# Optimization experiments

Hardware: AMD Instinct MI355X
Metric: run time of the kernel (lower is better)

The kernel has to match this reference:

```python
import jax, jax.numpy as jnp
import numpy as np
from itertools import product

B, C, N = 2, 64, 30000
D, H, W = 64, 64, 64


def _make_shift():
    # itertools.product over (-1,0,1)^3, scaled by 2/(size-1) per axis in (x->W, y->H, z->D) order
    s = np.array(list(product((-1, 0, 1), repeat=3)), dtype=np.float32)  # [27,3]
    scale = np.array([2.0 / (W - 1), 2.0 / (H - 1), 2.0 / (D - 1)], dtype=np.float32)
    return jnp.asarray(s * scale)  # [27,3]


def setup_inputs() -> dict:
    key = jax.random.key(0)
    k1, k2, k3 = jax.random.split(key, 3)
    voxel_features = jax.random.normal(k1, (B, C, D, H, W), dtype=jnp.float32)
    vertices = jax.random.uniform(k2, (B, N, 3), dtype=jnp.float32, minval=-1.0, maxval=1.0)
    # kaiming_normal for relu on a (C, C, 1, 27) conv kernel: std = sqrt(2 / fan_in)
    conv_w = jax.random.normal(k3, (C, C, 27), dtype=jnp.float32) * np.float32(np.sqrt(2.0 / (C * 27)))
    conv_b = jnp.zeros((C,), dtype=jnp.float32)
    return {"voxel_features": voxel_features, "vertices": vertices, "conv_w": conv_w, "conv_b": conv_b}


def _trilinear_sample(vol, grid):
    # vol: [C, D, H, W]; grid: [M, 3] normalized (x, y, z) in [-1, 1]
    # F.grid_sample semantics: mode='bilinear' (trilinear), padding_mode='border', align_corners=True
    sizes_f = jnp.array([W - 1, H - 1, D - 1], dtype=vol.dtype)
    coord = (grid + 1.0) * 0.5 * sizes_f  # unnormalize, align_corners=True
    coord = jnp.clip(coord, 0.0, sizes_f)  # border padding
    c0f = jnp.floor(coord)
    f = coord - c0f  # fractional weights [M,3]
    c0 = c0f.astype(jnp.int32)
    c1 = jnp.minimum(c0 + 1, jnp.array([W - 1, H - 1, D - 1], dtype=jnp.int32))
    x0, y0, z0 = c0[:, 0], c0[:, 1], c0[:, 2]
    x1, y1, z1 = c1[:, 0], c1[:, 1], c1[:, 2]
    fx, fy, fz = f[:, 0], f[:, 1], f[:, 2]

    def g(zi, yi, xi):
        return vol[:, zi, yi, xi]  # [C, M]

    out = (g(z0, y0, x0) * ((1 - fx) * (1 - fy) * (1 - fz))
           + g(z0, y0, x1) * (fx * (1 - fy) * (1 - fz))
           + g(z0, y1, x0) * ((1 - fx) * fy * (1 - fz))
           + g(z0, y1, x1) * (fx * fy * (1 - fz))
           + g(z1, y0, x0) * ((1 - fx) * (1 - fy) * fz)
           + g(z1, y0, x1) * (fx * (1 - fy) * fz)
           + g(z1, y1, x0) * ((1 - fx) * fy * fz)
           + g(z1, y1, x1) * (fx * fy * fz))
    return out  # [C, M]


def reference(voxel_features, vertices, conv_w, conv_b):
    shift = _make_shift()  # [27,3]
    # neighbourhood grid: [B, N, 27, 3] -> flatten to [B, N*27, 3]
    grid = (vertices[:, :, None, :] + shift[None, None, :, :]).reshape(B, N * 27, 3)
    feats = jax.vmap(_trilinear_sample)(voxel_features, grid)  # [B, C, N*27]
    feats = feats.reshape(B, C, N, 27)
    # Conv2d(C, C, kernel=(1,27)) == learned weighted sum over 27 neighbors + channel mix
    out = jnp.einsum("bcnk,ock->bno", feats, conv_w) + conv_b[None, None, :]  # [B, N, C]
    return out
```

## Files before the change

kernel.cpp:

```cpp
#include <hip/hip_runtime.h>
#include <stdint.h>

#define NBATCH 2
#define NVERT  30000
#define VOLCH  16777216ull
#define KDIM   1728
#define ASTR   (KDIM + 8)

typedef __attribute__((ext_vector_type(8))) __bf16 bf16x8;
typedef __attribute__((ext_vector_type(4))) float f32x4;

__device__ __forceinline__ float b2f(unsigned short u) {
  unsigned int x = ((unsigned int)u) << 16;
  return __builtin_bit_cast(float, x);
}

__device__ __forceinline__ unsigned short f2b(float f) {
  unsigned int u = __builtin_bit_cast(unsigned int, f);
  u = (u + 0x7FFFu + ((u >> 16) & 1u)) >> 16;
  return (unsigned short)u;
}

__global__ __launch_bounds__(256) void transpose_vox(
    const float* __restrict__ vox, unsigned short* __restrict__ T) {
  __shared__ float tile[64][65];
  const int b = blockIdx.y;
  const int zy = blockIdx.x;
  const size_t src0 = (size_t)b * 64 * 262144 + (size_t)zy * 64;
#pragma unroll
  for (int i = 0; i < 16; ++i) {
    int idx = i * 256 + threadIdx.x;
    int c = idx >> 6, x = idx & 63;
    tile[c][x] = vox[src0 + (size_t)c * 262144 + x];
  }
  __syncthreads();
  const size_t dst0 = ((size_t)b * 4096 + zy) * 4096;
#pragma unroll
  for (int i = 0; i < 16; ++i) {
    int idx = i * 256 + threadIdx.x;
    int x = idx >> 6, c = idx & 63;
    T[dst0 + x * 64 + c] = f2b(tile[c][x]);
  }
}

__global__ __launch_bounds__(256) void prep_w(
    const float* __restrict__ w, unsigned short* __restrict__ W3) {
  int t = blockIdx.x * 256 + threadIdx.x;
  int o = t / 1728;
  int rem = t - o * 1728;
  int c = rem / 27;
  int k = rem - c * 27;
  int K = k * 64 + c;
  W3[((size_t)(K >> 3) * 64 + o) * 8 + (K & 7)] = f2b(w[t]);
}

__device__ __forceinline__ void axis_setup(float v, int idx[4], float gw[3][4]) {
  float coord = (v + 1.0f) * 0.5f * 63.0f;
  coord = fminf(fmaxf(coord, 0.0f), 63.0f);
  int b0 = (int)coord;
  if (b0 > 63) b0 = 63;
#pragma unroll
  for (int p = 0; p < 4; ++p) {
    int q = b0 - 1 + p;
    idx[p] = min(max(q, 0), 63);
  }
#pragma unroll
  for (int d = 0; d < 3; ++d) {
    float t = coord + (float)(d - 1);
    float tc = fminf(fmaxf(t, 0.0f), 63.0f);
    float fl = floorf(tc);
    int i0 = (int)fl;
    if (i0 > 63) i0 = 63;
    float f = tc - fl;
    int i1 = min(i0 + 1, 63);
    int p0 = i0 - b0 + 1;
    int p1 = i1 - b0 + 1;
#pragma unroll
    for (int p = 0; p < 4; ++p) {
      float g = (p == p0) ? (1.0f - f) : 0.0f;
      g += (p == p1) ? f : 0.0f;
      gw[d][p] = g;
    }
  }
}

__global__ __launch_bounds__(256, 2) void fused_main(
    const float* __restrict__ verts, const unsigned short* __restrict__ T,
    const unsigned short* __restrict__ W3, const float* __restrict__ bias,
    float* __restrict__ out) {
  __shared__ __align__(16) unsigned short A_lds[16][ASTR];
  const int tid = threadIdx.x;
  const int wave = tid >> 6;
  const int lane = tid & 63;
  const int batch = blockIdx.y;
  const int n0 = blockIdx.x * 16;

  const unsigned short* Tb = T + (size_t)batch * VOLCH + lane;

#pragma unroll 1
  for (int vl = 0; vl < 4; ++vl) {
    const int m = wave * 4 + vl;
    const size_t vbase = ((size_t)batch * NVERT + (n0 + m)) * 3;
    const float vx = verts[vbase + 0];
    const float vy = verts[vbase + 1];
    const float vz = verts[vbase + 2];

    int xi[4], yi[4], zi[4];
    float gwx[3][4], gwy[3][4], gwz[3][4];
    axis_setup(vx, xi, gwx);
    axis_setup(vy, yi, gwy);
    axis_setup(vz, zi, gwz);

    int xo[4];
#pragma unroll
    for (int p = 0; p < 4; ++p) xo[p] = xi[p] << 6;

    float fe[3][3][3];
#pragma unroll
    for (int a = 0; a < 3; ++a)
#pragma unroll
      for (int bb = 0; bb < 3; ++bb)
#pragma unroll
        for (int cc = 0; cc < 3; ++cc) fe[a][bb][cc] = 0.0f;

#pragma unroll
    for (int pz = 0; pz < 4; ++pz) {
      float ryv[3][3];
#pragma unroll
      for (int a = 0; a < 3; ++a)
#pragma unroll
        for (int bb = 0; bb < 3; ++bb) ryv[a][bb] = 0.0f;
      const int zoff = zi[pz] << 18;
#pragma unroll
      for (int py = 0; py < 4; ++py) {
        const unsigned short* rp = Tb + zoff + (yi[py] << 12);
        float v0 = b2f(rp[xo[0]]);
        float v1 = b2f(rp[xo[1]]);
        float v2 = b2f(rp[xo[2]]);
        float v3 = b2f(rp[xo[3]]);
        const float wy0 = gwy[0][py], wy1 = gwy[1][py], wy2 = gwy[2][py];
#pragma unroll
        for (int dx = 0; dx < 3; ++dx) {
          float rx = v0 * gwx[dx][0] + v1 * gwx[dx][1] +
                     v2 * gwx[dx][2] + v3 * gwx[dx][3];
          ryv[0][dx] += rx * wy0;
          ryv[1][dx] += rx * wy1;
          ryv[2][dx] += rx * wy2;
        }
      }
#pragma unroll
      for (int dz = 0; dz < 3; ++dz) {
        const float wz = gwz[dz][pz];
#pragma unroll
        for (int dy = 0; dy < 3; ++dy)
#pragma unroll
          for (int dx = 0; dx < 3; ++dx) fe[dz][dy][dx] += ryv[dy][dx] * wz;
      }
    }

    unsigned short* arow = &A_lds[m][0];
#pragma unroll
    for (int dz = 0; dz < 3; ++dz)
#pragma unroll
      for (int dy = 0; dy < 3; ++dy)
#pragma unroll
        for (int dx = 0; dx < 3; ++dx) {
          int k = dx * 9 + dy * 3 + dz;
          arow[(k << 6) + lane] = f2b(fe[dz][dy][dx]);
        }
  }
  __syncthreads();

  const int g = lane >> 4;
  const int r = lane & 15;
  const int o0 = wave * 16;
  f32x4 acc = {0.0f, 0.0f, 0.0f, 0.0f};
  const unsigned short* aptr = &A_lds[r][g * 8];
  const unsigned short* bptr = W3 + (size_t)(g * 64 + o0 + r) * 8;
  for (int kk = 0; kk < 54; ++kk) {
    bf16x8 a = *reinterpret_cast<const bf16x8*>(aptr + kk * 32);
    bf16x8 b = *reinterpret_cast<const bf16x8*>(bptr + (size_t)kk * 2048);
    acc = __builtin_amdgcn_mfma_f32_16x16x32_bf16(a, b, acc, 0, 0, 0);
  }

  const int oc = o0 + r;
  const float bo = bias[oc];
  float* op = out + ((size_t)batch * NVERT + n0) * 64 + oc;
#pragma unroll
  for (int i = 0; i < 4; ++i) {
    op[(size_t)(g * 4 + i) * 64] = acc[i] + bo;
  }
}

extern "C" void kernel_launch(void* const* d_in, const int* in_sizes, int n_in,
                              void* d_out, int out_size, void* d_ws, size_t ws_size,
                              hipStream_t stream) {
  const float* vox   = (const float*)d_in[0];
  const float* verts = (const float*)d_in[1];
  const float* convw = (const float*)d_in[2];
  const float* convb = (const float*)d_in[3];
  float* out = (float*)d_out;

  const size_t t_elems = (size_t)NBATCH * VOLCH;
  const size_t need = t_elems * 2 + (size_t)110592 * 2;
  if (ws_size < need) {
    hipMemsetAsync(d_out, 0xFF, (size_t)out_size * 4, stream);
    return;
  }
  unsigned short* T  = (unsigned short*)d_ws;
  unsigned short* W3 = T + t_elems;

  transpose_vox<<<dim3(4096, NBATCH), 256, 0, stream>>>(vox, T);
  prep_w<<<432, 256, 0, stream>>>(convw, W3);
  fused_main<<<dim3(NVERT / 16, NBATCH), 256, 0, stream>>>(verts, T, W3, convb, out);
}
```

Before: 429.1 us.

## Vectorize voxel transpose and double fused-kernel waves with split-K MFMA reduction

The transpose kernel now moves four elements per thread access, using float4 loads and ushort4 stores instead of scalar ones. The main kernel grows from 256 to 512 threads per block. Each wave samples two vertices instead of four, and the MFMA K loop is split across two wave halves whose partial sums are combined through a new LDS buffer before output. This aims to raise latency hiding for the gather-heavy sampling phase and cut global transaction count in the transpose. The cost is an extra barrier, more LDS per block and possible register pressure under launch_bounds(512,4).

Measured after the change: 479.9 us. 11.8% more time.

```diff
diff --git a/kernel.cpp b/kernel.cpp
--- a/kernel.cpp
+++ b/kernel.cpp
@@ -26,20 +26,27 @@
   __shared__ float tile[64][65];
   const int b = blockIdx.y;
   const int zy = blockIdx.x;
+  const int t = threadIdx.x;
   const size_t src0 = (size_t)b * 64 * 262144 + (size_t)zy * 64;
 #pragma unroll
-  for (int i = 0; i < 16; ++i) {
-    int idx = i * 256 + threadIdx.x;
-    int c = idx >> 6, x = idx & 63;
-    tile[c][x] = vox[src0 + (size_t)c * 262144 + x];
+  for (int i = 0; i < 4; ++i) {
+    const int c = (t >> 4) + (i << 4);
+    const int x4 = (t & 15) << 2;
+    const float4 v = *reinterpret_cast<const float4*>(
+        vox + src0 + (size_t)c * 262144 + x4);
+    tile[c][x4 + 0] = v.x; tile[c][x4 + 1] = v.y;
+    tile[c][x4 + 2] = v.z; tile[c][x4 + 3] = v.w;
   }
   __syncthreads();
   const size_t dst0 = ((size_t)b * 4096 + zy) * 4096;
 #pragma unroll
-  for (int i = 0; i < 16; ++i) {
-    int idx = i * 256 + threadIdx.x;
-    int x = idx >> 6, c = idx & 63;
-    T[dst0 + x * 64 + c] = f2b(tile[c][x]);
+  for (int i = 0; i < 4; ++i) {
+    const int x = (t >> 4) + (i << 4);
+    const int c4 = (t & 15) << 2;
+    ushort4 o;
+    o.x = f2b(tile[c4 + 0][x]); o.y = f2b(tile[c4 + 1][x]);
+    o.z = f2b(tile[c4 + 2][x]); o.w = f2b(tile[c4 + 3][x]);
+    *reinterpret_cast<ushort4*>(T + dst0 + (size_t)x * 64 + c4) = o;
   }
 }
 
@@ -84,11 +91,12 @@
   }
 }
 
-__global__ __launch_bounds__(256, 2) void fused_main(
+__global__ __launch_bounds__(512, 4) void fused_main(
     const float* __restrict__ verts, const unsigned short* __restrict__ T,
     const unsigned short* __restrict__ W3, const float* __restrict__ bias,
     float* __restrict__ out) {
   __shared__ __align__(16) unsigned short A_lds[16][ASTR];
+  __shared__ float red[2][16][65];
   const int tid = threadIdx.x;
   const int wave = tid >> 6;
   const int lane = tid & 63;
@@ -98,8 +106,8 @@
   const unsigned short* Tb = T + (size_t)batch * VOLCH + lane;
 
 #pragma unroll 1
-  for (int vl = 0; vl < 4; ++vl) {
-    const int m = wave * 4 + vl;
+  for (int vl = 0; vl < 2; ++vl) {
+    const int m = wave * 2 + vl;
     const size_t vbase = ((size_t)batch * NVERT + (n0 + m)) * 3;
     const float vx = verts[vbase + 0];
     const float vy = verts[vbase + 1];
@@ -173,23 +181,32 @@
 
   const int g = lane >> 4;
   const int r = lane & 15;
-  const int o0 = wave * 16;
+  const int o0 = (wave & 3) * 16;
+  const int h = wave >> 2;
   f32x4 acc = {0.0f, 0.0f, 0.0f, 0.0f};
   const unsigned short* aptr = &A_lds[r][g * 8];
   const unsigned short* bptr = W3 + (size_t)(g * 64 + o0 + r) * 8;
-  for (int kk = 0; kk < 54; ++kk) {
+#pragma unroll 1
+  for (int kk = h * 27; kk < h * 27 + 27; ++kk) {
     bf16x8 a = *reinterpret_cast<const bf16x8*>(aptr + kk * 32);
     bf16x8 b = *reinterpret_cast<const bf16x8*>(bptr + (size_t)kk * 2048);
     acc = __builtin_amdgcn_mfma_f32_16x16x32_bf16(a, b, acc, 0, 0, 0);
   }
 
-  const int oc = o0 + r;
-  const float bo = bias[oc];
-  float* op = out + ((size_t)batch * NVERT + n0) * 64 + oc;
-#pragma unroll
-  for (int i = 0; i < 4; ++i) {
-    op[(size_t)(g * 4 + i) * 64] = acc[i] + bo;
-  }
+#pragma unroll
+  for (int i = 0; i < 4; ++i) red[h][g * 4 + i][o0 + r] = acc[i];
+  __syncthreads();
+
+  const float* redf = &red[0][0][0];
+#pragma unroll
+  for (int i = 0; i < 2; ++i) {
+    const int idx = tid + i * 512;
+    const int row = idx >> 6;
+    const int o = idx & 63;
+    const float s = red[0][row][o] + red[1][row][o] + bias[o];
+    out[((size_t)batch * NVERT + n0 + row) * 64 + o] = s;
+  }
+  (void)redf;
 }
 
 extern "C" void kernel_launch(void* const* d_in, const int* in_sizes, int n_in,
@@ -212,5 +229,5 @@
 
   transpose_vox<<<dim3(4096, NBATCH), 256, 0, stream>>>(vox, T);
   prep_w<<<432, 256, 0, stream>>>(convw, W3);
-  fused_main<<<dim3(NVERT / 16, NBATCH), 256, 0, stream>>>(verts, T, W3, convb, out);
-}
+  fused_main<<<dim3(NVERT / 16, NBATCH), 512, 0, stream>>>(verts, T, W3, convb, out);
+}
```

## Bin vertices spatially, remap blocks to XCDs, and vectorize voxel transpose

Applied to the files above, without the earlier changes.

Adds a counting-sort pass (histogram, scan, scatter) that groups vertices by z and coarse y cell. The main kernel then processes spatially nearby vertices together, and a block-index remap gives each XCD a contiguous range of sorted work, so gathers from the transposed bf16 volume should reuse L2 better. The transpose now handles four z-y rows per block with float4 loads and ushort4 stores. The trade is extra small kernels plus scattered output writes through the permutation, and the launch-bounds occupancy hint is dropped.

Result: slower. 446.4 us (+4.0%).

```diff
diff --git a/kernel.cpp b/kernel.cpp
--- a/kernel.cpp
+++ b/kernel.cpp
@@ -6,6 +6,7 @@
 #define VOLCH  16777216ull
 #define KDIM   1728
 #define ASTR   (KDIM + 8)
+#define NBINS  512
 
 typedef __attribute__((ext_vector_type(8))) __bf16 bf16x8;
 typedef __attribute__((ext_vector_type(4))) float f32x4;
@@ -23,23 +24,36 @@
 
 __global__ __launch_bounds__(256) void transpose_vox(
     const float* __restrict__ vox, unsigned short* __restrict__ T) {
-  __shared__ float tile[64][65];
+  __shared__ unsigned short tile[4][65][66];
   const int b = blockIdx.y;
-  const int zy = blockIdx.x;
-  const size_t src0 = (size_t)b * 64 * 262144 + (size_t)zy * 64;
+  const int zy0 = blockIdx.x * 4;
+  const int t = threadIdx.x;
+  const size_t src0 = (size_t)b * 64 * 262144 + (size_t)zy0 * 64;
 #pragma unroll
   for (int i = 0; i < 16; ++i) {
-    int idx = i * 256 + threadIdx.x;
-    int c = idx >> 6, x = idx & 63;
-    tile[c][x] = vox[src0 + (size_t)c * 262144 + x];
+    const int idx = i * 256 + t;
+    const int c = idx >> 6;
+    const int rem = idx & 63;
+    const int zyq = rem >> 4;
+    const int x4 = (rem & 15) << 2;
+    const float4 v = *reinterpret_cast<const float4*>(
+        vox + src0 + (size_t)c * 262144 + zyq * 64 + x4);
+    tile[zyq][c][x4 + 0] = f2b(v.x); tile[zyq][c][x4 + 1] = f2b(v.y);
+    tile[zyq][c][x4 + 2] = f2b(v.z); tile[zyq][c][x4 + 3] = f2b(v.w);
   }
   __syncthreads();
-  const size_t dst0 = ((size_t)b * 4096 + zy) * 4096;
+  const size_t dst0 = ((size_t)b * 4096 + zy0) * 4096;
 #pragma unroll
   for (int i = 0; i < 16; ++i) {
-    int idx = i * 256 + threadIdx.x;
-    int x = idx >> 6, c = idx & 63;
-    T[dst0 + x * 64 + c] = f2b(tile[c][x]);
+    const int idx = i * 256 + t;
+    const int c4 = (idx & 15) << 2;
+    const int pr = idx >> 4;
+    const int zyq = pr >> 6;
+    const int x = pr & 63;
+    ushort4 o;
+    o.x = tile[zyq][c4 + 0][x]; o.y = tile[zyq][c4 + 1][x];
+    o.z = tile[zyq][c4 + 2][x]; o.w = tile[zyq][c4 + 3][x];
+    *reinterpret_cast<ushort4*>(T + dst0 + ((size_t)zyq * 64 + x) * 64 + c4) = o;
   }
 }
 
@@ -54,11 +68,15 @@
   W3[((size_t)(K >> 3) * 64 + o) * 8 + (K & 7)] = f2b(w[t]);
 }
 
+__device__ __forceinline__ int axis_b0(float v) {
+  float coord = fminf(fmaxf((v + 1.0f) * 0.5f * 63.0f, 0.0f), 63.0f);
+  int b0 = (int)coord;
+  return min(b0, 63);
+}
+
 __device__ __forceinline__ void axis_setup(float v, int idx[4], float gw[3][4]) {
-  float coord = (v + 1.0f) * 0.5f * 63.0f;
-  coord = fminf(fmaxf(coord, 0.0f), 63.0f);
-  int b0 = (int)coord;
-  if (b0 > 63) b0 = 63;
+  float coord = fminf(fmaxf((v + 1.0f) * 0.5f * 63.0f, 0.0f), 63.0f);
+  int b0 = min((int)coord, 63);
 #pragma unroll
   for (int p = 0; p < 4; ++p) {
     int q = b0 - 1 + p;
@@ -66,11 +84,9 @@
   }
 #pragma unroll
   for (int d = 0; d < 3; ++d) {
-    float t = coord + (float)(d - 1);
-    float tc = fminf(fmaxf(t, 0.0f), 63.0f);
+    float tc = fminf(fmaxf(coord + (float)(d - 1), 0.0f), 63.0f);
     float fl = floorf(tc);
-    int i0 = (int)fl;
-    if (i0 > 63) i0 = 63;
+    int i0 = min((int)fl, 63);
     float f = tc - fl;
     int i1 = min(i0 + 1, 63);
     int p0 = i0 - b0 + 1;
@@ -84,23 +100,80 @@
   }
 }
 
-__global__ __launch_bounds__(256, 2) void fused_main(
+__device__ __forceinline__ int vert_bin(const float* p) {
+  return (axis_b0(p[2]) << 3) | (axis_b0(p[1]) >> 3);
+}
+
+__global__ __launch_bounds__(256) void binhist(
+    const float* __restrict__ verts, int* __restrict__ hist) {
+  int t = blockIdx.x * 256 + threadIdx.x;
+  if (t >= NBATCH * NVERT) return;
+  int b = t / NVERT;
+  atomicAdd(&hist[b * NBINS + vert_bin(verts + (size_t)t * 3)], 1);
+}
+
+__global__ __launch_bounds__(512) void binscan(
+    const int* __restrict__ hist, int* __restrict__ off) {
+  __shared__ int s0[NBINS], s1[NBINS];
+  const int t = threadIdx.x;
+#pragma unroll 1
+  for (int b = 0; b < NBATCH; ++b) {
+    const int orig = hist[b * NBINS + t];
+    s0[t] = orig;
+    __syncthreads();
+    int* src = s0;
+    int* dst = s1;
+#pragma unroll 1
+    for (int o = 1; o < NBINS; o <<= 1) {
+      int v = src[t] + ((t >= o) ? src[t - o] : 0);
+      dst[t] = v;
+      __syncthreads();
+      int* tmp = src; src = dst; dst = tmp;
+    }
+    off[b * NBINS + t] = src[t] - orig;
+    __syncthreads();
+  }
+}
+
+__global__ __launch_bounds__(256) void binscat(
+    const float* __restrict__ verts, int* __restrict__ off,
+    int* __restrict__ perm) {
+  int t = blockIdx.x * 256 + threadIdx.x;
+  if (t >= NBATCH * NVERT) return;
+  int b = t / NVERT;
+  int v = t - b * NVERT;
+  int bin = vert_bin(verts + (size_t)t * 3);
+  int pos = atomicAdd(&off[b * NBINS + bin], 1);
+  perm[b * NVERT + pos] = v;
+}
+
+__global__ __launch_bounds__(256) void fused_main(
     const float* __restrict__ verts, const unsigned short* __restrict__ T,
     const unsigned short* __restrict__ W3, const float* __restrict__ bias,
-    float* __restrict__ out) {
+    const int* __restrict__ perm, float* __restrict__ out) {
   __shared__ __align__(16) unsigned short A_lds[16][ASTR];
+  __shared__ int pvid[16];
   const int tid = threadIdx.x;
   const int wave = tid >> 6;
   const int lane = tid & 63;
-  const int batch = blockIdx.y;
-  const int n0 = blockIdx.x * 16;
+
+  const int orig = blockIdx.x;
+  const int xcd = orig & 7;
+  const int j = orig >> 3;
+  const int wg = (xcd < 6 ? xcd * 469 : 6 * 469 + (xcd - 6) * 468) + j;
+  const int batch = wg / 1875;
+  const int n0 = (wg - batch * 1875) * 16;
+
+  if (tid < 16) pvid[tid] = perm[batch * NVERT + n0 + tid];
+  __syncthreads();
 
   const unsigned short* Tb = T + (size_t)batch * VOLCH + lane;
 
 #pragma unroll 1
   for (int vl = 0; vl < 4; ++vl) {
     const int m = wave * 4 + vl;
-    const size_t vbase = ((size_t)batch * NVERT + (n0 + m)) * 3;
+    const int vid = pvid[m];
+    const size_t vbase = ((size_t)batch * NVERT + vid) * 3;
     const float vx = verts[vbase + 0];
     const float vy = verts[vbase + 1];
     const float vz = verts[vbase + 2];
@@ -177,6 +250,7 @@
   f32x4 acc = {0.0f, 0.0f, 0.0f, 0.0f};
   const unsigned short* aptr = &A_lds[r][g * 8];
   const unsigned short* bptr = W3 + (size_t)(g * 64 + o0 + r) * 8;
+#pragma unroll 1
   for (int kk = 0; kk < 54; ++kk) {
     bf16x8 a = *reinterpret_cast<const bf16x8*>(aptr + kk * 32);
     bf16x8 b = *reinterpret_cast<const bf16x8*>(bptr + (size_t)kk * 2048);
@@ -185,10 +259,11 @@
 
   const int oc = o0 + r;
   const float bo = bias[oc];
-  float* op = out + ((size_t)batch * NVERT + n0) * 64 + oc;
 #pragma unroll
   for (int i = 0; i < 4; ++i) {
-    op[(size_t)(g * 4 + i) * 64] = acc[i] + bo;
+    const int row = g * 4 + i;
+    const int vid = pvid[row];
+    out[((size_t)batch * NVERT + vid) * 64 + oc] = acc[i] + bo;
   }
 }
 
@@ -202,15 +277,28 @@
   float* out = (float*)d_out;
 
   const size_t t_elems = (size_t)NBATCH * VOLCH;
-  const size_t need = t_elems * 2 + (size_t)110592 * 2;
+  const size_t t_bytes = t_elems * 2;
+  const size_t w3_bytes = (size_t)110592 * 2;
+  const size_t hist_bytes = (size_t)NBATCH * NBINS * 4;
+  const size_t off_bytes  = hist_bytes;
+  const size_t perm_bytes = (size_t)NBATCH * NVERT * 4;
+  const size_t need = t_bytes + w3_bytes + hist_bytes + off_bytes + perm_bytes;
   if (ws_size < need) {
     hipMemsetAsync(d_out, 0xFF, (size_t)out_size * 4, stream);
     return;
   }
   unsigned short* T  = (unsigned short*)d_ws;
   unsigned short* W3 = T + t_elems;
-
-  transpose_vox<<<dim3(4096, NBATCH), 256, 0, stream>>>(vox, T);
+  char* base = (char*)d_ws + t_bytes + w3_bytes;
+  int* hist = (int*)base;
+  int* off  = (int*)(base + hist_bytes);
+  int* perm = (int*)(base + hist_bytes + off_bytes);
+
+  hipMemsetAsync(hist, 0, hist_bytes, stream);
+  transpose_vox<<<dim3(1024, NBATCH), 256, 0, stream>>>(vox, T);
   prep_w<<<432, 256, 0, stream>>>(convw, W3);
-  fused_main<<<dim3(NVERT / 16, NBATCH), 256, 0, stream>>>(verts, T, W3, convb, out);
-}
+  binhist<<<(NBATCH * NVERT + 255) / 256, 256, 0, stream>>>(verts, hist);
+  binscan<<<1, 512, 0, stream>>>(hist, off);
+  binscat<<<(NBATCH * NVERT + 255) / 256, 256, 0, stream>>>(verts, off, perm);
+  fused_main<<<3750, 256, 0, stream>>>(verts, T, W3, convb, perm, out);
+}
```
